# Performance work log

Measured on AMD Instinct MI355X. Metric: run time of the kernel, lower is better.

## Reference

```python
import jax, jax.numpy as jnp
import numpy as np

H = 51  # hidden size hardcoded in the module

def _lstm_cell(x, h, c, W_ih, W_hh, b_ih, b_hh):
    # PyTorch LSTMCell: gates ordered (i, f, g, o)
    z = x @ W_ih.T + h @ W_hh.T + b_ih + b_hh  # [B, 4H]
    i, f, g, o = jnp.split(z, 4, axis=-1)
    i = jax.nn.sigmoid(i)
    f = jax.nn.sigmoid(f)
    g = jnp.tanh(g)
    o = jax.nn.sigmoid(o)
    c_new = f * c + i * g
    h_new = o * jnp.tanh(c_new)
    return h_new, c_new

def setup_inputs() -> dict:
    key = jax.random.key(0)
    ks = jax.random.split(key, 12)
    B, T = 512, 512
    s = 1.0 / np.sqrt(H)  # PyTorch default init scale
    def u(k, shape):
        return jax.random.uniform(k, shape, jnp.float32, -s, s)
    return {
        "input": jax.random.normal(ks[0], (B, T), jnp.float32),
        "W_ih1": u(ks[1], (4 * H, 1)),
        "W_hh1": u(ks[2], (4 * H, H)),
        "b_ih1": u(ks[3], (4 * H,)),
        "b_hh1": u(ks[4], (4 * H,)),
        "W_ih2": u(ks[5], (4 * H, H)),
        "W_hh2": u(ks[6], (4 * H, H)),
        "b_ih2": u(ks[7], (4 * H,)),
        "b_hh2": u(ks[8], (4 * H,)),
        "W_lin": u(ks[9], (1, H)),
        "b_lin": u(ks[10], (1,)),
        "future": 0,
    }

def reference(input, W_ih1, W_hh1, b_ih1, b_hh1, W_ih2, W_hh2, b_ih2, b_hh2, W_lin, b_lin, future):
    B, T = input.shape
    h1 = jnp.zeros((B, H), input.dtype)
    c1 = jnp.zeros((B, H), input.dtype)
    h2 = jnp.zeros((B, H), input.dtype)
    c2 = jnp.zeros((B, H), input.dtype)

    def step(carry, x_t):
        h1, c1, h2, c2 = carry
        h1, c1 = _lstm_cell(x_t, h1, c1, W_ih1, W_hh1, b_ih1, b_hh1)
        h2, c2 = _lstm_cell(h1, h2, c2, W_ih2, W_hh2, b_ih2, b_hh2)
        out = h2 @ W_lin.T + b_lin  # [B, 1]
        return (h1, c1, h2, c2), out

    xs = jnp.transpose(input)[:, :, None]  # [T, B, 1]
    carry, outs = jax.lax.scan(step, (h1, c1, h2, c2), xs)
    outputs = jnp.transpose(outs[:, :, 0])  # [B, T]

    if future > 0:
        last = outs[-1]  # [B, 1]

        def fstep(carry, _):
            state, x = carry
            state, out = step(state, x)
            return (state, out), out

        _, fouts = jax.lax.scan(fstep, (carry, last), None, length=future)
        outputs = jnp.concatenate([outputs, jnp.transpose(fouts[:, :, 0])], axis=1)
    return outputs
```

## Files before the change

### kernel.cpp

```cpp
#include <hip/hip_runtime.h>

#define Hh 51
#define TT 512
#define MR 2
#define NBLK 256
#define BT 512
#define SHR 80
#define NIT 514
#define LOG2E 1.4426950408889634f

typedef _Float16 half8 __attribute__((ext_vector_type(8)));
typedef __attribute__((ext_vector_type(4))) float f32x4;

__device__ __forceinline__ float fexp2(float x){ return __builtin_amdgcn_exp2f(x); }
__device__ __forceinline__ float frcp(float x){ return __builtin_amdgcn_rcpf(x); }
__device__ __forceinline__ unsigned short h16bits(_Float16 h){
    union { _Float16 h; unsigned short u; } c; c.h = h; return c.u;
}
__device__ __forceinline__ unsigned packhl(float v){
    _Float16 hi = (_Float16)v;
    _Float16 lo = (_Float16)(v - (float)hi);
    return (unsigned)h16bits(hi) | ((unsigned)h16bits(lo) << 16);
}

__device__ __forceinline__ float lstm_update(float vg0, float vg1, float vg2,
                                             float vg3, float& cst){
    float e_i = fexp2(vg0);
    float e_f = fexp2(vg1);
    float e_g = fexp2(vg2);
    float e_o = fexp2(vg3);
    float a_i = e_i + 1.f, a_f = e_f + 1.f;
    float gp  = e_g + 1.f, gm = e_g - 1.f, a_o = e_o + 1.f;
    float u  = a_i * gp;
    float N  = fmaf(cst, u, gm * a_f);
    float rD = frcp(a_f * u);
    cst = N * rD;
    float zc2 = fminf(2.f * LOG2E * cst, 60.f);
    float e_c = fexp2(zc2);
    float r2  = frcp((e_c + 1.f) * a_o);
    return (e_c - 1.f) * r2;
}

#define MFMAH(a,b,c) __builtin_amdgcn_mfma_f32_16x16x32_f16(a,b,c,0,0,0)

__global__ __launch_bounds__(BT, 2) void lstm2_fold(
    const float* __restrict__ input,
    const float* __restrict__ W_ih1,
    const float* __restrict__ W_hh1,
    const float* __restrict__ b_ih1,
    const float* __restrict__ b_hh1,
    const float* __restrict__ W_ih2,
    const float* __restrict__ W_hh2,
    const float* __restrict__ b_ih2,
    const float* __restrict__ b_hh2,
    const float* __restrict__ W_lin,
    const float* __restrict__ b_lin,
    float* __restrict__ out)
{
    __shared__ unsigned xsp[(TT+1)*MR];
    __shared__ float ob[TT*MR];
    __shared__ __align__(16) _Float16 H1[2][16*SHR];
    __shared__ __align__(16) _Float16 H2[2][16*SHR];

    const int tid  = threadIdx.x;
    const int wv   = tid >> 6;
    const int lane = tid & 63;
    const int quad = lane >> 4;
    const int n16  = lane & 15;
    const int row0 = blockIdx.x * MR;
    const bool g1  = (wv < 4);
    const bool w3  = (wv == 3);
    const int  w   = g1 ? wv : (wv - 4);
    const int  l   = 13 * w + n16;
    const bool valid = (n16 <= 12) && (l < Hh);
    const bool liveA = ((n16 & 11) == 0);
    const bool updL  = (quad < MR) && valid;
    const bool xw    = (wv == 0) && (n16 == 0) && (quad < MR);
    const int  fo    = n16 * SHR + quad * 8;
    const int  ho    = (quad * 4) * SHR + l;

#pragma unroll
    for (int i = 0; i < MR; ++i) {
        int idx = i * BT + tid; int m = idx >> 9, t = idx & 511;
        xsp[t * MR + m] = packhl(input[(row0 + m) * TT + t]);
    }
    if (tid < MR) xsp[TT * MR + tid] = 0u;
    for (int i = tid; i < 2 * 16 * SHR / 2; i += BT) {
        ((int*)H1)[i] = 0; ((int*)H2)[i] = 0;
    }

    half8 z8 = {0,0,0,0,0,0,0,0};
    half8 B1[4][2];
    half8 B2[4][2], B3[4][2];
    half8 Bout[2];
    const f32x4 zc = (f32x4){0.f,0.f,0.f,0.f};
#pragma unroll
    for (int gt = 0; gt < 4; ++gt) {
        const float gs = (gt == 2) ? (2.f * LOG2E) : (-LOG2E);
        int jrow = gt * Hh + l;
        float bias = 0.f, wih = 0.f;
        if (valid) {
            bias = gs * (g1 ? (b_ih1[jrow] + b_hh1[jrow]) : (b_ih2[jrow] + b_hh2[jrow]));
            wih  = g1 ? (gs * W_ih1[jrow]) : 0.f;
        }
        _Float16 bhi = (_Float16)bias;
        _Float16 blo = (_Float16)(bias - (float)bhi);
        _Float16 wih_h = (_Float16)wih;
#pragma unroll
        for (int kt = 0; kt < 2; ++kt) {
            B1[gt][kt] = z8; B2[gt][kt] = z8; B3[gt][kt] = z8;
#pragma unroll
            for (int jj = 0; jj < 8; ++jj) {
                int k = kt * 32 + quad * 8 + jj;
                if (valid) {
                    if (g1) {
                        if (k < Hh)       B1[gt][kt][jj] = (_Float16)(gs * W_hh1[jrow * Hh + k]);
                        else if (k == 51) B1[gt][kt][jj] = bhi;
                        else if (k == 52 || k == 53) B1[gt][kt][jj] = wih_h;
                        else if (k == 54) B1[gt][kt][jj] = blo;
                    } else {
                        if (k < Hh) {
                            B2[gt][kt][jj] = (_Float16)(gs * W_ih2[jrow * Hh + k]);
                            B3[gt][kt][jj] = (_Float16)(gs * W_hh2[jrow * Hh + k]);
                        } else if (k == 51) B2[gt][kt][jj] = bhi;
                        else if (k == 54)   B2[gt][kt][jj] = blo;
                    }
                }
            }
        }
    }
    {
        float blf = b_lin[0];
        _Float16 blhi = (_Float16)blf;
        _Float16 bllo = (_Float16)(blf - (float)blhi);
#pragma unroll
        for (int kt = 0; kt < 2; ++kt) {
            Bout[kt] = z8;
#pragma unroll
            for (int jj = 0; jj < 8; ++jj) {
                int k = kt * 32 + quad * 8 + jj;
                if (w3 && n16 == 0) {
                    if (k < Hh)       Bout[kt][jj] = (_Float16)W_lin[k];
                    else if (k == 51) Bout[kt][jj] = blhi;
                    else if (k == 54) Bout[kt][jj] = bllo;
                }
            }
        }
    }
    float cst = 0.f;

    half8 f1a = z8, f1b = z8;
    half8 f2a = z8, f2b = z8;

    __syncthreads();
    if (tid < MR) {
        int r = tid * 4 * SHR;
#pragma unroll
        for (int p = 0; p < 2; ++p) {
            H1[p][r + 51] = (_Float16)1.0f;  H1[p][r + 54] = (_Float16)1.0f;
            H2[p][r + 51] = (_Float16)1.0f;  H2[p][r + 54] = (_Float16)1.0f;
        }
        *(unsigned*)&H1[1][r + 52] = xsp[tid];
    }
    __syncthreads();

    auto stepfn = [&](int n, int pA, int pB) {
        if (g1) {
            if (w3 && n >= 2) {
                if (liveA) {
                    f2a = *(const half8*)&H2[pB][fo];
                    f2b = *(const half8*)&H2[pB][fo + 32];
                }
            }
            if (n < TT) {
                unsigned xn = xw ? xsp[(n + 1) * MR + quad] : 0u;
                if (liveA) {
                    f1a = *(const half8*)&H1[pA][fo];
                    f1b = *(const half8*)&H1[pA][fo + 32];
                }
                f32x4 ac[4];
#pragma unroll
                for (int gt = 0; gt < 4; ++gt) {
                    f32x4 a = MFMAH(f1a, B1[gt][0], zc);
                    a       = MFMAH(f1b, B1[gt][1], a);
                    ac[gt] = a;
                }
                if (updL) {
                    float h = lstm_update(ac[0][0], ac[1][0], ac[2][0], ac[3][0], cst);
                    H1[pB][ho] = (_Float16)h;
                }
                if (xw) *(unsigned*)&H1[pB][(quad * 4) * SHR + 52] = xn;
            }
            if (w3 && n >= 2) {
                f32x4 ao = MFMAH(f2a, Bout[0], zc);
                ao       = MFMAH(f2b, Bout[1], ao);
                if (n16 == 0 && quad < MR) ob[(n - 2) * MR + quad] = ao[0];
            }
        } else if (n >= 1 && n <= TT) {
            if (liveA) {
                f1a = *(const half8*)&H1[pA][fo];
                f1b = *(const half8*)&H1[pA][fo + 32];
                f2a = *(const half8*)&H2[pB][fo];
                f2b = *(const half8*)&H2[pB][fo + 32];
            }
            float vg[4];
#pragma unroll
            for (int gt = 0; gt < 4; ++gt) {
                f32x4 m2 = MFMAH(f2a, B3[gt][0], zc);
                m2       = MFMAH(f2b, B3[gt][1], m2);
                f32x4 m1 = MFMAH(f1a, B2[gt][0], zc);
                m1       = MFMAH(f1b, B2[gt][1], m1);
                vg[gt] = m2[0] + m1[0];
            }
            if (updL) {
                float h = lstm_update(vg[0], vg[1], vg[2], vg[3], cst);
                H2[pA][ho] = (_Float16)h;
            }
        }
        __syncthreads();
    };

    for (int k2 = 0; k2 < NIT / 2; ++k2) {
        stepfn(2 * k2,     1, 0);
        stepfn(2 * k2 + 1, 0, 1);
    }

#pragma unroll
    for (int i = 0; i < MR; ++i) {
        int idx = i * BT + tid; int m = idx >> 9, t = idx & 511;
        out[(row0 + m) * TT + t] = ob[t * MR + m];
    }
}

extern "C" void kernel_launch(void* const* d_in, const int* in_sizes, int n_in,
                              void* d_out, int out_size, void* d_ws, size_t ws_size,
                              hipStream_t stream) {
    const float* input = (const float*)d_in[0];
    const float* W_ih1 = (const float*)d_in[1];
    const float* W_hh1 = (const float*)d_in[2];
    const float* b_ih1 = (const float*)d_in[3];
    const float* b_hh1 = (const float*)d_in[4];
    const float* W_ih2 = (const float*)d_in[5];
    const float* W_hh2 = (const float*)d_in[6];
    const float* b_ih2 = (const float*)d_in[7];
    const float* b_hh2 = (const float*)d_in[8];
    const float* W_lin = (const float*)d_in[9];
    const float* b_lin = (const float*)d_in[10];
    float* out = (float*)d_out;

    hipLaunchKernelGGL(lstm2_fold, dim3(NBLK), dim3(BT), 0, stream,
                       input, W_ih1, W_hh1, b_ih1, b_hh1,
                       W_ih2, W_hh2, b_ih2, b_hh2, W_lin, b_lin, out);
}
```

Measured before the change: 280.8 us.

## Merge layer-1 and layer-2 wave groups so each wave computes both LSTM layers

Halves the block from 8 waves to 4. Each wave now owns 13 hidden units of both layers, holding B1, B2 and B3 weights and two cell states, instead of splitting waves into a layer-1 group and a layer-2 group. The goal is cheaper per-step __syncthreads with fewer waves and better balance, since the layer-1 waves had less MFMA work than the layer-2 waves. The cost is serialised per-wave work, because each wave runs both layers back to back, plus higher register pressure. Occupancy hint drops to 1 block.

```diff
diff --git a/kernel.cpp b/kernel.cpp
--- a/kernel.cpp
+++ b/kernel.cpp
@@ -4,7 +4,7 @@
 #define TT 512
 #define MR 2
 #define NBLK 256
-#define BT 512
+#define BT 256
 #define SHR 80
 #define NIT 514
 #define LOG2E 1.4426950408889634f
@@ -43,7 +43,7 @@
 
 #define MFMAH(a,b,c) __builtin_amdgcn_mfma_f32_16x16x32_f16(a,b,c,0,0,0)
 
-__global__ __launch_bounds__(BT, 2) void lstm2_fold(
+__global__ __launch_bounds__(BT, 1) void lstm2_fold(
     const float* __restrict__ input,
     const float* __restrict__ W_ih1,
     const float* __restrict__ W_hh1,
@@ -68,10 +68,8 @@
     const int quad = lane >> 4;
     const int n16  = lane & 15;
     const int row0 = blockIdx.x * MR;
-    const bool g1  = (wv < 4);
     const bool w3  = (wv == 3);
-    const int  w   = g1 ? wv : (wv - 4);
-    const int  l   = 13 * w + n16;
+    const int  l   = 13 * wv + n16;
     const bool valid = (n16 <= 12) && (l < Hh);
     const bool liveA = ((n16 & 11) == 0);
     const bool updL  = (quad < MR) && valid;
@@ -79,9 +77,8 @@
     const int  fo    = n16 * SHR + quad * 8;
     const int  ho    = (quad * 4) * SHR + l;
 
-#pragma unroll
-    for (int i = 0; i < MR; ++i) {
-        int idx = i * BT + tid; int m = idx >> 9, t = idx & 511;
+    for (int idx = tid; idx < TT * MR; idx += BT) {
+        int m = idx >> 9, t = idx & 511;
         xsp[t * MR + m] = packhl(input[(row0 + m) * TT + t]);
     }
     if (tid < MR) xsp[TT * MR + tid] = 0u;
@@ -98,13 +95,16 @@
     for (int gt = 0; gt < 4; ++gt) {
         const float gs = (gt == 2) ? (2.f * LOG2E) : (-LOG2E);
         int jrow = gt * Hh + l;
-        float bias = 0.f, wih = 0.f;
+        float b1 = 0.f, b2 = 0.f, wih = 0.f;
         if (valid) {
-            bias = gs * (g1 ? (b_ih1[jrow] + b_hh1[jrow]) : (b_ih2[jrow] + b_hh2[jrow]));
-            wih  = g1 ? (gs * W_ih1[jrow]) : 0.f;
-        }
-        _Float16 bhi = (_Float16)bias;
-        _Float16 blo = (_Float16)(bias - (float)bhi);
+            b1  = gs * (b_ih1[jrow] + b_hh1[jrow]);
+            b2  = gs * (b_ih2[jrow] + b_hh2[jrow]);
+            wih = gs * W_ih1[jrow];
+        }
+        _Float16 b1hi = (_Float16)b1;
+        _Float16 b1lo = (_Float16)(b1 - (float)b1hi);
+        _Float16 b2hi = (_Float16)b2;
+        _Float16 b2lo = (_Float16)(b2 - (float)b2hi);
         _Float16 wih_h = (_Float16)wih;
 #pragma unroll
         for (int kt = 0; kt < 2; ++kt) {
@@ -113,17 +113,16 @@
             for (int jj = 0; jj < 8; ++jj) {
                 int k = kt * 32 + quad * 8 + jj;
                 if (valid) {
-                    if (g1) {
-                        if (k < Hh)       B1[gt][kt][jj] = (_Float16)(gs * W_hh1[jrow * Hh + k]);
-                        else if (k == 51) B1[gt][kt][jj] = bhi;
-                        else if (k == 52 || k == 53) B1[gt][kt][jj] = wih_h;
-                        else if (k == 54) B1[gt][kt][jj] = blo;
-                    } else {
-                        if (k < Hh) {
-                            B2[gt][kt][jj] = (_Float16)(gs * W_ih2[jrow * Hh + k]);
-                            B3[gt][kt][jj] = (_Float16)(gs * W_hh2[jrow * Hh + k]);
-                        } else if (k == 51) B2[gt][kt][jj] = bhi;
-                        else if (k == 54)   B2[gt][kt][jj] = blo;
+                    if (k < Hh) {
+                        B1[gt][kt][jj] = (_Float16)(gs * W_hh1[jrow * Hh + k]);
+                        B2[gt][kt][jj] = (_Float16)(gs * W_ih2[jrow * Hh + k]);
+                        B3[gt][kt][jj] = (_Float16)(gs * W_hh2[jrow * Hh + k]);
+                    } else if (k == 51) {
+                        B1[gt][kt][jj] = b1hi;  B2[gt][kt][jj] = b2hi;
+                    } else if (k == 52 || k == 53) {
+                        B1[gt][kt][jj] = wih_h;
+                    } else if (k == 54) {
+                        B1[gt][kt][jj] = b1lo;  B2[gt][kt][jj] = b2lo;
                     }
                 }
             }
@@ -147,7 +146,7 @@
             }
         }
     }
-    float cst = 0.f;
+    float cst1 = 0.f, cst2 = 0.f;
 
     half8 f1a = z8, f1b = z8;
     half8 f2a = z8, f2b = z8;
@@ -165,44 +164,13 @@
     __syncthreads();
 
     auto stepfn = [&](int n, int pA, int pB) {
-        if (g1) {
-            if (w3 && n >= 2) {
-                if (liveA) {
-                    f2a = *(const half8*)&H2[pB][fo];
-                    f2b = *(const half8*)&H2[pB][fo + 32];
-                }
-            }
-            if (n < TT) {
-                unsigned xn = xw ? xsp[(n + 1) * MR + quad] : 0u;
-                if (liveA) {
-                    f1a = *(const half8*)&H1[pA][fo];
-                    f1b = *(const half8*)&H1[pA][fo + 32];
-                }
-                f32x4 ac[4];
-#pragma unroll
-                for (int gt = 0; gt < 4; ++gt) {
-                    f32x4 a = MFMAH(f1a, B1[gt][0], zc);
-                    a       = MFMAH(f1b, B1[gt][1], a);
-                    ac[gt] = a;
-                }
-                if (updL) {
-                    float h = lstm_update(ac[0][0], ac[1][0], ac[2][0], ac[3][0], cst);
-                    H1[pB][ho] = (_Float16)h;
-                }
-                if (xw) *(unsigned*)&H1[pB][(quad * 4) * SHR + 52] = xn;
-            }
-            if (w3 && n >= 2) {
-                f32x4 ao = MFMAH(f2a, Bout[0], zc);
-                ao       = MFMAH(f2b, Bout[1], ao);
-                if (n16 == 0 && quad < MR) ob[(n - 2) * MR + quad] = ao[0];
-            }
-        } else if (n >= 1 && n <= TT) {
-            if (liveA) {
-                f1a = *(const half8*)&H1[pA][fo];
-                f1b = *(const half8*)&H1[pA][fo + 32];
-                f2a = *(const half8*)&H2[pB][fo];
-                f2b = *(const half8*)&H2[pB][fo + 32];
-            }
+        if (liveA) {
+            f1a = *(const half8*)&H1[pA][fo];
+            f1b = *(const half8*)&H1[pA][fo + 32];
+            f2a = *(const half8*)&H2[pB][fo];
+            f2b = *(const half8*)&H2[pB][fo + 32];
+        }
+        if (n >= 1 && n <= TT) {
             float vg[4];
 #pragma unroll
             for (int gt = 0; gt < 4; ++gt) {
@@ -213,9 +181,29 @@
                 vg[gt] = m2[0] + m1[0];
             }
             if (updL) {
-                float h = lstm_update(vg[0], vg[1], vg[2], vg[3], cst);
+                float h = lstm_update(vg[0], vg[1], vg[2], vg[3], cst2);
                 H2[pA][ho] = (_Float16)h;
             }
+        }
+        if (n < TT) {
+            unsigned xn = xw ? xsp[(n + 1) * MR + quad] : 0u;
+            float vg[4];
+#pragma unroll
+            for (int gt = 0; gt < 4; ++gt) {
+                f32x4 a = MFMAH(f1a, B1[gt][0], zc);
+                a       = MFMAH(f1b, B1[gt][1], a);
+                vg[gt] = a[0];
+            }
+            if (updL) {
+                float h = lstm_update(vg[0], vg[1], vg[2], vg[3], cst1);
+                H1[pB][ho] = (_Float16)h;
+            }
+            if (xw) *(unsigned*)&H1[pB][(quad * 4) * SHR + 52] = xn;
+        }
+        if (w3 && n >= 2) {
+            f32x4 ao = MFMAH(f2a, Bout[0], zc);
+            ao       = MFMAH(f2b, Bout[1], ao);
+            if (n16 == 0 && quad < MR) ob[(n - 2) * MR + quad] = ao[0];
         }
         __syncthreads();
     };
@@ -225,9 +213,8 @@
         stepfn(2 * k2 + 1, 0, 1);
     }
 
-#pragma unroll
-    for (int i = 0; i < MR; ++i) {
-        int idx = i * BT + tid; int m = idx >> 9, t = idx & 511;
+    for (int idx = tid; idx < TT * MR; idx += BT) {
+        int m = idx >> 9, t = idx & 511;
         out[(row0 + m) * TT + t] = ob[t * MR + m];
     }
 }
```

Measured after the change: 367.0 us. 1.31x slower.

## Break MFMA accumulation chains, simplify LSTM gate math, prioritize layer-2 waves

Applied to the files above, without the earlier changes.

Each pair of chained MFMAs becomes two independent MFMAs summed on the VALU, which shortens the dependent latency chain on the serial recurrence critical path. The fused-rational LSTM update is rewritten as separate reciprocal-based sigmoids and tanh, and the fminf clamp on the cell exponent is dropped. Layer-2 waves get raised scheduling priority, and their H2 loads are issued first. This trades a few extra VALU adds and reciprocals for lower MFMA dependency latency, and the unclamped exp could hit inf, though the rcp form still returns the correct limit.

```diff
diff --git a/kernel.cpp b/kernel.cpp
--- a/kernel.cpp
+++ b/kernel.cpp
@@ -25,20 +25,14 @@
 
 __device__ __forceinline__ float lstm_update(float vg0, float vg1, float vg2,
                                              float vg3, float& cst){
-    float e_i = fexp2(vg0);
-    float e_f = fexp2(vg1);
-    float e_g = fexp2(vg2);
-    float e_o = fexp2(vg3);
-    float a_i = e_i + 1.f, a_f = e_f + 1.f;
-    float gp  = e_g + 1.f, gm = e_g - 1.f, a_o = e_o + 1.f;
-    float u  = a_i * gp;
-    float N  = fmaf(cst, u, gm * a_f);
-    float rD = frcp(a_f * u);
-    cst = N * rD;
-    float zc2 = fminf(2.f * LOG2E * cst, 60.f);
-    float e_c = fexp2(zc2);
-    float r2  = frcp((e_c + 1.f) * a_o);
-    return (e_c - 1.f) * r2;
+    float ei = fexp2(vg0), ef = fexp2(vg1), eg = fexp2(vg2), eo = fexp2(vg3);
+    float ii = frcp(1.f + ei);
+    float ff = frcp(1.f + ef);
+    float gg = fmaf(-2.f, frcp(1.f + eg), 1.f);
+    float oo = frcp(1.f + eo);
+    cst = fmaf(ff, cst, ii * gg);
+    float r  = frcp(1.f + fexp2(2.f * LOG2E * cst));
+    return fmaf(-2.f * oo, r, oo);
 }
 
 #define MFMAH(a,b,c) __builtin_amdgcn_mfma_f32_16x16x32_f16(a,b,c,0,0,0)
@@ -178,44 +172,46 @@
                     f1a = *(const half8*)&H1[pA][fo];
                     f1b = *(const half8*)&H1[pA][fo + 32];
                 }
-                f32x4 ac[4];
+                float vg[4];
 #pragma unroll
                 for (int gt = 0; gt < 4; ++gt) {
-                    f32x4 a = MFMAH(f1a, B1[gt][0], zc);
-                    a       = MFMAH(f1b, B1[gt][1], a);
-                    ac[gt] = a;
+                    f32x4 m0 = MFMAH(f1a, B1[gt][0], zc);
+                    f32x4 m1 = MFMAH(f1b, B1[gt][1], zc);
+                    vg[gt] = m0[0] + m1[0];
                 }
                 if (updL) {
-                    float h = lstm_update(ac[0][0], ac[1][0], ac[2][0], ac[3][0], cst);
+                    float h = lstm_update(vg[0], vg[1], vg[2], vg[3], cst);
                     H1[pB][ho] = (_Float16)h;
                 }
                 if (xw) *(unsigned*)&H1[pB][(quad * 4) * SHR + 52] = xn;
             }
             if (w3 && n >= 2) {
-                f32x4 ao = MFMAH(f2a, Bout[0], zc);
-                ao       = MFMAH(f2b, Bout[1], ao);
-                if (n16 == 0 && quad < MR) ob[(n - 2) * MR + quad] = ao[0];
+                f32x4 o0 = MFMAH(f2a, Bout[0], zc);
+                f32x4 o1 = MFMAH(f2b, Bout[1], zc);
+                if (n16 == 0 && quad < MR) ob[(n - 2) * MR + quad] = o0[0] + o1[0];
             }
         } else if (n >= 1 && n <= TT) {
+            __builtin_amdgcn_s_setprio(1);
             if (liveA) {
+                f2a = *(const half8*)&H2[pB][fo];
+                f2b = *(const half8*)&H2[pB][fo + 32];
                 f1a = *(const half8*)&H1[pA][fo];
                 f1b = *(const half8*)&H1[pA][fo + 32];
-                f2a = *(const half8*)&H2[pB][fo];
-                f2b = *(const half8*)&H2[pB][fo + 32];
             }
             float vg[4];
 #pragma unroll
             for (int gt = 0; gt < 4; ++gt) {
-                f32x4 m2 = MFMAH(f2a, B3[gt][0], zc);
-                m2       = MFMAH(f2b, B3[gt][1], m2);
-                f32x4 m1 = MFMAH(f1a, B2[gt][0], zc);
-                m1       = MFMAH(f1b, B2[gt][1], m1);
-                vg[gt] = m2[0] + m1[0];
+                f32x4 m0 = MFMAH(f2a, B3[gt][0], zc);
+                f32x4 m1 = MFMAH(f2b, B3[gt][1], zc);
+                f32x4 m2 = MFMAH(f1a, B2[gt][0], zc);
+                f32x4 m3 = MFMAH(f1b, B2[gt][1], zc);
+                vg[gt] = (m0[0] + m1[0]) + (m2[0] + m3[0]);
             }
             if (updL) {
                 float h = lstm_update(vg[0], vg[1], vg[2], vg[3], cst);
                 H2[pA][ho] = (_Float16)h;
             }
+            __builtin_amdgcn_s_setprio(0);
         }
         __syncthreads();
     };
```

Result: slower. 326.6 us (+16.3%).
